# Performance work log

Hardware: AMD Instinct MI355X
Metric: run time of the kernel (lower is better)

The kernel has to match this reference:

```python
import jax, jax.numpy as jnp
import numpy as np

N_NODES = 15000
N_EDGES = 40000
N_GRAPHS = 750
D = 64
NODE_DIM = 32
EDGE_DIM = 16
NUM_CONV = 3
S2S_STEPS = 3


def setup_inputs() -> dict:
    key = jax.random.key(0)
    ks = jax.random.split(key, 24)
    s = 0.05
    inp = {
        'x': jax.random.normal(ks[0], (N_NODES, NODE_DIM), jnp.float32),
        'edge_attr': jax.random.uniform(ks[1], (N_EDGES, EDGE_DIM), jnp.float32),
        'edge_index': jax.random.randint(ks[2], (2, N_EDGES), 0, N_NODES),
        'batch': jnp.sort(jax.random.randint(ks[3], (N_NODES,), 0, N_GRAPHS)),
        # input projection
        'in_W': jax.random.normal(ks[4], (NODE_DIM, D)) * s,
        'in_b': jnp.zeros((D,)),
        # edge MLP -> per-edge DxD weights
        'e1_W': jax.random.normal(ks[5], (EDGE_DIM, D)) * s,
        'e1_b': jnp.zeros((D,)),
        'e2_W': jax.random.normal(ks[6], (D, D * D)) * s,
        'e2_b': jnp.zeros((D * D,)),
        'conv_b': jnp.zeros((D,)),
        # GRU (gate order r,z,n like torch)
        'gru_Wih': jax.random.normal(ks[7], (3 * D, D)) * s,
        'gru_Whh': jax.random.normal(ks[8], (3 * D, D)) * s,
        'gru_bih': jnp.zeros((3 * D,)),
        'gru_bhh': jnp.zeros((3 * D,)),
        # Set2Set LSTM (gate order i,f,g,o like torch), input 2D -> hidden D
        'lstm_Wih': jax.random.normal(ks[9], (4 * D, 2 * D)) * s,
        'lstm_Whh': jax.random.normal(ks[10], (4 * D, D)) * s,
        'lstm_bih': jnp.zeros((4 * D,)),
        'lstm_bhh': jnp.zeros((4 * D,)),
        # output MLP
        'out1_W': jax.random.normal(ks[11], (2 * D, 2 * D)) * s,
        'out1_b': jnp.zeros((2 * D,)),
        'out2_W': jax.random.normal(ks[12], (2 * D, 1)) * s,
        'out2_b': jnp.zeros((1,)),
    }
    return inp


def _gru_cell(m, h, Wih, Whh, bih, bhh):
    gi = m @ Wih.T + bih
    gh = h @ Whh.T + bhh
    ir, iz, inn = jnp.split(gi, 3, axis=-1)
    hr, hz, hn = jnp.split(gh, 3, axis=-1)
    r = jax.nn.sigmoid(ir + hr)
    z = jax.nn.sigmoid(iz + hz)
    n = jnp.tanh(inn + r * hn)
    return (1.0 - z) * n + z * h


def _lstm_cell(q, h, c, Wih, Whh, bih, bhh):
    g = q @ Wih.T + bih + h @ Whh.T + bhh
    i, f, gg, o = jnp.split(g, 4, axis=-1)
    c = jax.nn.sigmoid(f) * c + jax.nn.sigmoid(i) * jnp.tanh(gg)
    h = jax.nn.sigmoid(o) * jnp.tanh(c)
    return h, c


def reference(x, edge_attr, edge_index, batch,
              in_W, in_b, e1_W, e1_b, e2_W, e2_b, conv_b,
              gru_Wih, gru_Whh, gru_bih, gru_bhh,
              lstm_Wih, lstm_Whh, lstm_bih, lstm_bhh,
              out1_W, out1_b, out2_W, out2_b):
    src, dst = edge_index[0], edge_index[1]
    out = jax.nn.relu(x @ in_W + in_b)           # [N, D]
    h = out
    # edge-conditioned weights (edge_attr is constant across conv iters)
    W_e = (jax.nn.relu(edge_attr @ e1_W + e1_b) @ e2_W + e2_b).reshape(-1, D, D)  # [E, D, D]
    deg = jnp.maximum(jax.ops.segment_sum(jnp.ones((N_EDGES,), out.dtype), dst, N_NODES), 1.0)
    for _ in range(NUM_CONV):
        msg = jnp.einsum('ed,edf->ef', out[src], W_e)          # per-edge matmul
        agg = jax.ops.segment_sum(msg, dst, N_NODES) / deg[:, None]  # scatter-mean
        m = jax.nn.relu(agg + conv_b)
        h = _gru_cell(m, h, gru_Wih, gru_Whh, gru_bih, gru_bhh)
        out = h
    # Set2Set pooling
    q_star = jnp.zeros((N_GRAPHS, 2 * D), out.dtype)
    hl = jnp.zeros((N_GRAPHS, D), out.dtype)
    cl = jnp.zeros((N_GRAPHS, D), out.dtype)
    for _ in range(S2S_STEPS):
        hl, cl = _lstm_cell(q_star, hl, cl, lstm_Wih, lstm_Whh, lstm_bih, lstm_bhh)
        q = hl
        e = jnp.sum(out * q[batch], axis=-1)                    # [N]
        e = e - jax.ops.segment_max(e, batch, N_GRAPHS)[batch]
        ee = jnp.exp(e)
        a = ee / jax.ops.segment_sum(ee, batch, N_GRAPHS)[batch]
        r = jax.ops.segment_sum(a[:, None] * out, batch, N_GRAPHS)  # [G, D]
        q_star = jnp.concatenate([q, r], axis=-1)
    z = jax.nn.relu(q_star @ out1_W + out1_b) @ out2_W + out2_b
    return z
```

## Files before the change

### kernel.cpp

```cpp
#include <hip/hip_runtime.h>
#include <math.h>

#define N_NODES 15000
#define N_EDGES 40000
#define N_GRAPHS 750
#define N_TILES 938
#define N_TILES_PAD 944

typedef __attribute__((ext_vector_type(8))) short bf16x8;
typedef __attribute__((ext_vector_type(4))) float f32x4;

__device__ __forceinline__ float sigmoidf_(float x) { return 1.f / (1.f + expf(-x)); }

__device__ __forceinline__ unsigned short f2bf(float v) {
    unsigned u = __float_as_uint(v);
    unsigned r = (u + 0x7FFFu + ((u >> 16) & 1u)) >> 16;
    return (unsigned short)r;
}
__device__ __forceinline__ float bf2f(unsigned short b) {
    return __uint_as_float(((unsigned)b) << 16);
}


__global__ void tscan_kernel(const int* __restrict__ tcnt, int* __restrict__ tptr,
                             int* __restrict__ cursor) {
    __shared__ int buf[1024];
    int t = threadIdx.x;
    int v = (t < N_TILES) ? tcnt[t] : 0;
    buf[t] = v;
    __syncthreads();
    for (int ofs = 1; ofs < 1024; ofs <<= 1) {
        int a = (t >= ofs) ? buf[t - ofs] : 0;
        __syncthreads();
        buf[t] += a;
        __syncthreads();
    }
    int excl = buf[t] - v;
    if (t <= N_TILES_PAD) tptr[t] = excl;
    if (t < N_TILES) cursor[t] = excl;
}

__global__ void fillpack_kernel(const int* __restrict__ src, int* __restrict__ cursor,
                                int* __restrict__ edge_list,
                                const float* __restrict__ node_h,
                                unsigned short* __restrict__ Apack) {
    int b = blockIdx.x;
    int tid = threadIdx.x;
    if (b < 157) {
        int e = b * 256 + tid;
        if (e < N_EDGES) {
            int slot = atomicAdd(&cursor[src[e] >> 4], 1);
            edge_list[slot] = e;
        }
    } else {
        int nt = b - 157;
        for (int idx = tid; idx < 1024; idx += 256) {
            int kt = idx >> 9, lane = (idx >> 3) & 63, j = idx & 7;
            int quad = lane >> 4, m = lane & 15;
            int n = nt * 16 + m;
            float v = (n < N_NODES) ? node_h[(size_t)n * 64 + kt * 32 + quad * 8 + j] : 0.f;
            unsigned short hi = f2bf(v);
            Apack[nt * 2048 + kt * 1024 + lane * 8 + j] = hi;
            Apack[nt * 2048 + kt * 1024 + 512 + lane * 8 + j] = f2bf(v - bf2f(hi));
        }
    }
}

__global__ __launch_bounds__(256)
void prep_kernel(const float* __restrict__ x, const float* __restrict__ in_W,
                 const float* __restrict__ in_b, float* __restrict__ node_h,
                 const float* __restrict__ e2b,
                 const float* __restrict__ ea, const float* __restrict__ e1_W,
                 const float* __restrict__ e1_b, float* __restrict__ h1,
                 const float* __restrict__ e2W,
                 unsigned short* __restrict__ Bhi, unsigned short* __restrict__ Blo,
                 const float* __restrict__ lWih, const float* __restrict__ lWhh,
                 const float* __restrict__ gWih, const float* __restrict__ gWhh,
                 float* __restrict__ lWihT, float* __restrict__ lWhhT,
                 unsigned short* __restrict__ gWihP, unsigned short* __restrict__ gWhhP,
                 const int* __restrict__ batch, int* __restrict__ gptr,
                 const int* __restrict__ src, const int* __restrict__ dst,
                 int* __restrict__ tcnt, float* __restrict__ deg) {
    int b = blockIdx.x;
    int tid = threadIdx.x;
    if (b < 3750) {
        __shared__ float xs[4][32];
        int n0 = b * 4;
        if (tid < 128) xs[tid >> 5][tid & 31] = x[n0 * 32 + tid];
        __syncthreads();
        int nn = tid >> 6, f = tid & 63;
        float s = in_b[f];
        #pragma unroll
        for (int i = 0; i < 32; ++i) s += xs[nn][i] * in_W[i * 64 + f];
        node_h[(size_t)(n0 + nn) * 64 + f] = fmaxf(s, 0.f);
    } else if (b < 13750) {
        __shared__ float eas[4][16];
        int e0 = (b - 3750) * 4;
        if (tid < 64) eas[tid >> 4][tid & 15] = ea[e0 * 16 + tid];
        __syncthreads();
        int nn = tid >> 6, f = tid & 63;
        float s = e1_b[f];
        #pragma unroll
        for (int i = 0; i < 16; ++i) s += eas[nn][i] * e1_W[i * 64 + f];
        h1[(size_t)(e0 + nn) * 64 + f] = fmaxf(s, 0.f);
    } else if (b < 14806) {
        int idx = (b - 13750) * 256 + tid;
        int j = idx & 7, lane = (idx >> 3) & 63, kt = (idx >> 9) & 1;
        int rem = idx >> 10;
        int ct = rem % 33, ft = rem / 33;
        int d = kt * 32 + ((lane >> 4) << 3) + j;
        int m = lane & 15;
        float v;
        if (ct < 32) {
            int c = ct * 16 + m;
            int kk = c >> 3, fi = c & 7;
            v = e2W[(size_t)kk * 4096 + d * 64 + ft * 8 + fi];
        } else {
            v = (m < 8) ? e2b[d * 64 + ft * 8 + m] : 0.f;
        }
        unsigned short hi = f2bf(v);
        Bhi[idx] = hi;
        Blo[idx] = f2bf(v - bf2f(hi));
    } else if (b < 14998) {
        int idx = (b - 14806) * 256 + tid;
        if (idx < 32768) {
            int i = idx >> 8, r = idx & 255;
            lWihT[i * 256 + r] = lWih[r * 128 + i];
        } else if (idx < 49152) {
            int x2 = idx - 32768; int i = x2 >> 8, r = x2 & 255;
            lWhhT[i * 256 + r] = lWhh[r * 64 + i];
        }
    } else if (b < 15094) {
        int idx = (b - 14998) * 256 + tid;
        if (idx < 12288) {
            int j = idx & 7, lane = (idx >> 3) & 63, kt = (idx >> 9) & 1, ct = idx >> 10;
            int k = kt * 32 + ((lane >> 4) << 3) + j;
            int n = ct * 16 + (lane & 15);
            float v = gWih[n * 64 + k];
            unsigned short hi = f2bf(v);
            gWihP[idx] = hi;
            gWihP[12288 + idx] = f2bf(v - bf2f(hi));
        } else {
            int i2 = idx - 12288;
            int j = i2 & 7, lane = (i2 >> 3) & 63, kt = (i2 >> 9) & 1, ct = i2 >> 10;
            int k = kt * 32 + ((lane >> 4) << 3) + j;
            int n = ct * 16 + (lane & 15);
            float v = gWhh[n * 64 + k];
            unsigned short hi = f2bf(v);
            gWhhP[i2] = hi;
            gWhhP[12288 + i2] = f2bf(v - bf2f(hi));
        }
    } else if (b < 15153) {
        int n = (b - 15094) * 256 + tid;
        if (n < N_NODES) {
            int bb = batch[n];
            int pb = (n == 0) ? -1 : batch[n - 1];
            for (int g = pb + 1; g <= bb; ++g) gptr[g] = n;
            if (n == N_NODES - 1)
                for (int g = bb + 1; g <= N_GRAPHS; ++g) gptr[g] = N_NODES;
        }
    } else {
        int e = (b - 15153) * 256 + tid;
        if (e < N_EDGES) {
            atomicAdd(&tcnt[src[e] >> 4], 1);
            atomicAdd(&deg[dst[e]], 1.f);
        }
    }
}

__global__ __launch_bounds__(256, 4)
void conv_kernel(const unsigned short* __restrict__ Apack, const float* __restrict__ h1,
                 const unsigned short* __restrict__ Bhi, const unsigned short* __restrict__ Blo,
                 const int* __restrict__ tptr, const int* __restrict__ edge_list,
                 const int* __restrict__ src, const int* __restrict__ dst,
                 float* __restrict__ agg) {
    __shared__ float T_lds[16 * 548];
    int bid = blockIdx.x;
    int nt = bid % N_TILES_PAD, ft = bid / N_TILES_PAD;
    int n0 = nt * 16;
    int tid = threadIdx.x;
    int lane = tid & 63, wave = tid >> 6;
    int quad = lane >> 4, m = lane & 15;

    const unsigned short* ap = Apack + nt * 2048 + lane * 8;
    bf16x8 ahi[2], alo[2];
    ahi[0] = *(const bf16x8*)(ap);
    alo[0] = *(const bf16x8*)(ap + 512);
    ahi[1] = *(const bf16x8*)(ap + 1024);
    alo[1] = *(const bf16x8*)(ap + 1536);

    size_t base0 = (size_t)(ft * 33 + wave) * 1024 + lane * 8;
    const unsigned short* ph = Bhi + base0;
    const unsigned short* pl = Blo + base0;
    bf16x8 bh0 = *(const bf16x8*)(ph);
    bf16x8 bh1 = *(const bf16x8*)(ph + 512);
    bf16x8 bl0 = *(const bf16x8*)(pl);
    bf16x8 bl1 = *(const bf16x8*)(pl + 512);

    int nct = (wave == 0) ? 9 : 8;
    #pragma unroll 1
    for (int ci = 0; ci < nct; ++ci) {
        bf16x8 ch0 = bh0, ch1 = bh1, cl0 = bl0, cl1 = bl1;
        if (ci + 1 < nct) {
            const unsigned short* nh = ph + (size_t)(ci + 1) * 4096;
            const unsigned short* nl = pl + (size_t)(ci + 1) * 4096;
            bh0 = *(const bf16x8*)(nh);
            bh1 = *(const bf16x8*)(nh + 512);
            bl0 = *(const bf16x8*)(nl);
            bl1 = *(const bf16x8*)(nl + 512);
        }
        f32x4 accA = {0.f, 0.f, 0.f, 0.f};
        f32x4 accB = {0.f, 0.f, 0.f, 0.f};
        accA = __builtin_amdgcn_mfma_f32_16x16x32_bf16(ahi[0], ch0, accA, 0, 0, 0);
        accB = __builtin_amdgcn_mfma_f32_16x16x32_bf16(ahi[1], ch1, accB, 0, 0, 0);
        accA = __builtin_amdgcn_mfma_f32_16x16x32_bf16(alo[0], ch0, accA, 0, 0, 0);
        accB = __builtin_amdgcn_mfma_f32_16x16x32_bf16(alo[1], ch1, accB, 0, 0, 0);
        accA = __builtin_amdgcn_mfma_f32_16x16x32_bf16(ahi[0], cl0, accA, 0, 0, 0);
        accB = __builtin_amdgcn_mfma_f32_16x16x32_bf16(ahi[1], cl1, accB, 0, 0, 0);
        int ct = wave + ci * 4;
        int c = ct * 16 + m;
        int kk = c >> 3, fi = c & 7;
        #pragma unroll
        for (int r = 0; r < 4; ++r)
            T_lds[(quad * 4 + r) * 548 + fi * 68 + kk] = accA[r] + accB[r];
    }
    __syncthreads();

    int fi = tid & 7, slot = tid >> 3;
    int te0 = tptr[nt], te1 = tptr[nt + 1];
    for (int c = te0 + slot; c < te1; c += 64) {
        int c1 = c + 32;
        bool h2 = (c1 < te1);
        int e0 = edge_list[c];
        int e1 = h2 ? edge_list[c1] : e0;
        int nn0 = src[e0] - n0, nn1 = src[e1] - n0;
        const float* h0p = h1 + (size_t)e0 * 64;
        const float* h1p = h1 + (size_t)e1 * 64;
        const float* T0 = &T_lds[nn0 * 548 + fi * 68];
        const float* T1 = &T_lds[nn1 * 548 + fi * 68];
        float p00 = T0[64], p01 = 0.f;
        float p10 = T1[64], p11 = 0.f;
        #pragma unroll
        for (int k4 = 0; k4 < 64; k4 += 8) {
            float4 ha = *(const float4*)(h0p + k4);
            float4 ta = *(const float4*)(T0 + k4);
            float4 hb = *(const float4*)(h0p + k4 + 4);
            float4 tb = *(const float4*)(T0 + k4 + 4);
            float4 hc = *(const float4*)(h1p + k4);
            float4 tc = *(const float4*)(T1 + k4);
            float4 hd = *(const float4*)(h1p + k4 + 4);
            float4 td = *(const float4*)(T1 + k4 + 4);
            p00 += ha.x * ta.x + ha.y * ta.y + ha.z * ta.z + ha.w * ta.w;
            p01 += hb.x * tb.x + hb.y * tb.y + hb.z * tb.z + hb.w * tb.w;
            p10 += hc.x * tc.x + hc.y * tc.y + hc.z * tc.z + hc.w * tc.w;
            p11 += hd.x * td.x + hd.y * td.y + hd.z * td.z + hd.w * td.w;
        }
        atomicAdd(&agg[(size_t)dst[e0] * 64 + ft * 8 + fi], p00 + p01);
        if (h2) atomicAdd(&agg[(size_t)dst[e1] * 64 + ft * 8 + fi], p10 + p11);
    }
}

__global__ __launch_bounds__(256, 4)
void gru_kernel(float* __restrict__ node_h, float* __restrict__ agg,
                const float* __restrict__ deg, const float* __restrict__ conv_b,
                const unsigned short* __restrict__ WihP, const unsigned short* __restrict__ WhhP,
                const float* __restrict__ bih, const float* __restrict__ bhh,
                unsigned short* __restrict__ Apack, int want_pack) {
    __shared__ unsigned short m_bf[2][32][72];
    __shared__ unsigned short h_bf[2][32][72];
    __shared__ float h_s[32][68];
    __shared__ float hn_s[32][68];
    int n0 = blockIdx.x * 32;
    int tid = threadIdx.x;
    int lane = tid & 63, w = tid >> 6;
    int quad = lane >> 4, m16 = lane & 15;

    for (int i = tid; i < 2048; i += 256) {
        int c = i >> 6, f = i & 63;
        int n = n0 + c;
        float mv = 0.f, hv = 0.f;
        if (n < N_NODES) {
            float dg = fmaxf(deg[n], 1.f);
            mv = fmaxf(agg[(size_t)n * 64 + f] / dg + conv_b[f], 0.f);
            agg[(size_t)n * 64 + f] = 0.f;
            hv = node_h[(size_t)n * 64 + f];
        }
        unsigned short mh = f2bf(mv);
        m_bf[0][c][f] = mh; m_bf[1][c][f] = f2bf(mv - bf2f(mh));
        unsigned short hh = f2bf(hv);
        h_bf[0][c][f] = hh; h_bf[1][c][f] = f2bf(hv - bf2f(hh));
        h_s[c][f] = hv;
    }

    bf16x8 Bi[3][2][2], Bh[3][2][2];
    #pragma unroll
    for (int g = 0; g < 3; ++g)
        #pragma unroll
        for (int kt = 0; kt < 2; ++kt) {
            size_t base = ((size_t)((g * 4 + w) * 2 + kt) * 64 + lane) * 8;
            Bi[g][kt][0] = *(const bf16x8*)(WihP + base);
            Bi[g][kt][1] = *(const bf16x8*)(WihP + 12288 + base);
            Bh[g][kt][0] = *(const bf16x8*)(WhhP + base);
            Bh[g][kt][1] = *(const bf16x8*)(WhhP + 12288 + base);
        }
    int f = w * 16 + m16;
    float br_i = bih[f],       br_h = bhh[f];
    float bz_i = bih[64 + f],  bz_h = bhh[64 + f];
    float bn_i = bih[128 + f], bn_h = bhh[128 + f];
    __syncthreads();

    #pragma unroll 1
    for (int mt = 0; mt < 2; ++mt) {
        bf16x8 Am[2][2], Ah[2][2];
        #pragma unroll
        for (int kt = 0; kt < 2; ++kt) {
            Am[kt][0] = *(const bf16x8*)(&m_bf[0][mt * 16 + m16][kt * 32 + quad * 8]);
            Am[kt][1] = *(const bf16x8*)(&m_bf[1][mt * 16 + m16][kt * 32 + quad * 8]);
            Ah[kt][0] = *(const bf16x8*)(&h_bf[0][mt * 16 + m16][kt * 32 + quad * 8]);
            Ah[kt][1] = *(const bf16x8*)(&h_bf[1][mt * 16 + m16][kt * 32 + quad * 8]);
        }
        f32x4 ai[3], ah[3];
        #pragma unroll
        for (int g = 0; g < 3; ++g) { ai[g] = (f32x4){0.f,0.f,0.f,0.f}; ah[g] = (f32x4){0.f,0.f,0.f,0.f}; }
        #pragma unroll
        for (int g = 0; g < 3; ++g)
            #pragma unroll
            for (int kt = 0; kt < 2; ++kt) {
                ai[g] = __builtin_amdgcn_mfma_f32_16x16x32_bf16(Am[kt][0], Bi[g][kt][0], ai[g], 0, 0, 0);
                ai[g] = __builtin_amdgcn_mfma_f32_16x16x32_bf16(Am[kt][0], Bi[g][kt][1], ai[g], 0, 0, 0);
                ai[g] = __builtin_amdgcn_mfma_f32_16x16x32_bf16(Am[kt][1], Bi[g][kt][0], ai[g], 0, 0, 0);
                ah[g] = __builtin_amdgcn_mfma_f32_16x16x32_bf16(Ah[kt][0], Bh[g][kt][0], ah[g], 0, 0, 0);
                ah[g] = __builtin_amdgcn_mfma_f32_16x16x32_bf16(Ah[kt][0], Bh[g][kt][1], ah[g], 0, 0, 0);
                ah[g] = __builtin_amdgcn_mfma_f32_16x16x32_bf16(Ah[kt][1], Bh[g][kt][0], ah[g], 0, 0, 0);
            }
        #pragma unroll
        for (int r = 0; r < 4; ++r) {
            int node = mt * 16 + quad * 4 + r;
            float rr = sigmoidf_(ai[0][r] + br_i + ah[0][r] + br_h);
            float zz = sigmoidf_(ai[1][r] + bz_i + ah[1][r] + bz_h);
            float n2 = tanhf(ai[2][r] + bn_i + rr * (ah[2][r] + bn_h));
            float hnew = (1.f - zz) * n2 + zz * h_s[node][f];
            int n = n0 + node;
            if (n < N_NODES) node_h[(size_t)n * 64 + f] = hnew;
            hn_s[node][f] = hnew;
        }
    }
    if (want_pack) {
        __syncthreads();
        for (int idx = tid; idx < 2048; idx += 256) {
            int tt = idx >> 10, r2 = idx & 1023;
            int kt = r2 >> 9, ln = (r2 >> 3) & 63, j = r2 & 7;
            int q2 = ln >> 4, mm = ln & 15;
            float v = hn_s[tt * 16 + mm][kt * 32 + q2 * 8 + j];
            unsigned short hi = f2bf(v);
            size_t base = (size_t)(blockIdx.x * 2 + tt) * 2048 + kt * 1024 + ln * 8 + j;
            Apack[base] = hi;
            Apack[base + 512] = f2bf(v - bf2f(hi));
        }
    }
}

__global__ __launch_bounds__(128)
void s2s_kernel(const float* __restrict__ node_h, const int* __restrict__ gptr,
                const float* __restrict__ WihT, const float* __restrict__ WhhT,
                const float* __restrict__ bih, const float* __restrict__ bhh,
                const float* __restrict__ o1W, const float* __restrict__ o1b,
                const float* __restrict__ o2W, const float* __restrict__ o2b,
                float* __restrict__ z) {
    int g = blockIdx.x, tid = threadIdx.x;
    int f = tid & 63, half = tid >> 6;
    __shared__ float qs[128], hs[64], q[64], wts[128], gvs[4][64], racc_s[2][64];
    __shared__ float mred[2], sred[2], ored[2];
    if (half == 0) { qs[f] = 0.f; qs[64 + f] = 0.f; hs[f] = 0.f; }
    float c_t = 0.f;
    int nbeg = gptr[g], nend = gptr[g + 1];
    __syncthreads();
    for (int st = 0; st < 3; ++st) {
        #pragma unroll
        for (int gg = 0; gg < 2; ++gg) {
            int gate = half * 2 + gg;
            int row = gate * 64 + f;
            float s = bih[row] + bhh[row];
            #pragma unroll 8
            for (int i = 0; i < 128; ++i) s += qs[i] * WihT[i * 256 + row];
            #pragma unroll 8
            for (int i = 0; i < 64; ++i) s += hs[i] * WhhT[i * 256 + row];
            gvs[gate][f] = s;
        }
        __syncthreads();
        if (half == 0) {
            float c = sigmoidf_(gvs[1][f]) * c_t + sigmoidf_(gvs[0][f]) * tanhf(gvs[2][f]);
            float hn = sigmoidf_(gvs[3][f]) * tanhf(c);
            c_t = c;
            hs[f] = hn; q[f] = hn;
        }
        __syncthreads();
        float rm = -INFINITY, rs = 0.f, raccl = 0.f;
        for (int base = nbeg; base < nend; base += 128) {
            int n = base + tid;
            float e = -INFINITY;
            if (n < nend) {
                float s = 0.f;
                #pragma unroll 8
                for (int ff = 0; ff < 64; ++ff) s += node_h[(size_t)n * 64 + ff] * q[ff];
                e = s;
            }
            float cm = e;
            #pragma unroll
            for (int o = 32; o > 0; o >>= 1) cm = fmaxf(cm, __shfl_down(cm, o));
            if ((tid & 63) == 0) mred[half] = cm;
            __syncthreads();
            float bm = fmaxf(mred[0], mred[1]);
            float nm = fmaxf(rm, bm);
            float scale = (rm == -INFINITY) ? 0.f : expf(rm - nm);
            float wv = (n < nend) ? expf(e - nm) : 0.f;
            wts[tid] = wv;
            float cs = wv;
            #pragma unroll
            for (int o = 32; o > 0; o >>= 1) cs += __shfl_down(cs, o);
            if ((tid & 63) == 0) sred[half] = cs;
            __syncthreads();
            float bs = sred[0] + sred[1];
            float na = raccl * scale;
            int cnt2 = min(128, nend - base);
            int l0 = half * 64, l1 = min(l0 + 64, cnt2);
            for (int l = l0; l < l1; ++l) na += wts[l] * node_h[(size_t)(base + l) * 64 + f];
            raccl = na;
            rs = rs * scale + bs;
            rm = nm;
            __syncthreads();
        }
        racc_s[half][f] = raccl;
        __syncthreads();
        if (half == 0) {
            float r = (nend > nbeg) ? (racc_s[0][f] + racc_s[1][f]) / rs : 0.f;
            qs[f] = q[f];
            qs[64 + f] = r;
        }
        __syncthreads();
    }
    float sA = o1b[tid];
    #pragma unroll 8
    for (int i = 0; i < 128; ++i) sA += qs[i] * o1W[i * 128 + tid];
    float red = fmaxf(sA, 0.f) * o2W[tid];
    #pragma unroll
    for (int o = 32; o > 0; o >>= 1) red += __shfl_down(red, o);
    if ((tid & 63) == 0) ored[half] = red;
    __syncthreads();
    if (tid == 0) z[g] = ored[0] + ored[1] + o2b[0];
}

extern "C" void kernel_launch(void* const* d_in, const int* in_sizes, int n_in,
                              void* d_out, int out_size, void* d_ws, size_t ws_size,
                              hipStream_t stream) {
    const float* x         = (const float*)d_in[0];
    const float* edge_attr = (const float*)d_in[1];
    const int*   ei        = (const int*)d_in[2];
    const int*   batch     = (const int*)d_in[3];
    const float* in_W      = (const float*)d_in[4];
    const float* in_b      = (const float*)d_in[5];
    const float* e1_W      = (const float*)d_in[6];
    const float* e1_b      = (const float*)d_in[7];
    const float* e2_W      = (const float*)d_in[8];
    const float* e2_b      = (const float*)d_in[9];
    const float* conv_b    = (const float*)d_in[10];
    const float* gWih      = (const float*)d_in[11];
    const float* gWhh      = (const float*)d_in[12];
    const float* gbih      = (const float*)d_in[13];
    const float* gbhh      = (const float*)d_in[14];
    const float* lWih      = (const float*)d_in[15];
    const float* lWhh      = (const float*)d_in[16];
    const float* lbih      = (const float*)d_in[17];
    const float* lbhh      = (const float*)d_in[18];
    const float* o1W       = (const float*)d_in[19];
    const float* o1b       = (const float*)d_in[20];
    const float* o2W       = (const float*)d_in[21];
    const float* o2b       = (const float*)d_in[22];
    const int* src = ei;
    const int* dst = ei + N_EDGES;
    float* z = (float*)d_out;

    char* ws = (char*)d_ws;
    size_t off = 0;
    auto alloc = [&](size_t bytes) {
        void* p = ws + off;
        off = (off + bytes + 255) & ~(size_t)255;
        return p;
    };
    float* node_h   = (float*)alloc((size_t)N_NODES * 64 * 4);
    float* agg      = (float*)alloc((size_t)N_NODES * 64 * 4);
    float* h1       = (float*)alloc((size_t)N_EDGES * 64 * 4);
    unsigned short* Bhi = (unsigned short*)alloc((size_t)270336 * 2);
    unsigned short* Blo = (unsigned short*)alloc((size_t)270336 * 2);
    unsigned short* Apack = (unsigned short*)alloc((size_t)N_TILES_PAD * 2048 * 2);
    float* lWihT    = (float*)alloc(128 * 256 * 4);
    float* lWhhT    = (float*)alloc(64 * 256 * 4);
    unsigned short* gWihP = (unsigned short*)alloc(24576 * 2);
    unsigned short* gWhhP = (unsigned short*)alloc(24576 * 2);
    float* deg      = (float*)alloc(N_NODES * 4);
    int*   tcnt     = (int*)alloc((N_TILES + 2) * 4);
    int*   tcursor  = (int*)alloc((N_TILES + 2) * 4);
    int*   tptr     = (int*)alloc((N_TILES_PAD + 2) * 4);
    int*   edge_list= (int*)alloc(N_EDGES * 4);
    int*   gptr     = (int*)alloc((N_GRAPHS + 1) * 4);

    size_t degpad = ((size_t)N_NODES * 4 + 255) & ~(size_t)255;
    hipMemsetAsync(deg, 0, degpad + (N_TILES + 2) * 4, stream);
    hipMemsetAsync(agg, 0, (size_t)N_NODES * 64 * 4, stream);

    prep_kernel<<<15310, 256, 0, stream>>>(x, in_W, in_b, node_h, e2_b,
                                           edge_attr, e1_W, e1_b, h1,
                                           e2_W, Bhi, Blo,
                                           lWih, lWhh, gWih, gWhh,
                                           lWihT, lWhhT, gWihP, gWhhP,
                                           batch, gptr, src, dst, tcnt, deg);
    tscan_kernel<<<1, 1024, 0, stream>>>(tcnt, tptr, tcursor);
    fillpack_kernel<<<157 + N_TILES_PAD, 256, 0, stream>>>(src, tcursor, edge_list,
                                                           node_h, Apack);

    for (int it = 0; it < 3; ++it) {
        conv_kernel<<<N_TILES_PAD * 8, 256, 0, stream>>>(Apack, h1, Bhi, Blo,
                                                         tptr, edge_list, src, dst, agg);
        gru_kernel<<<469, 256, 0, stream>>>(node_h, agg, deg, conv_b,
                                            gWihP, gWhhP, gbih, gbhh,
                                            Apack, (it < 2) ? 1 : 0);
    }
    s2s_kernel<<<N_GRAPHS, 128, 0, stream>>>(node_h, gptr, lWihT, lWhhT, lbih, lbhh,
                                             o1W, o1b, o2W, o2b, z);
}
```

Before: 437.0 us.

## Prefetch first edge batch in conv, batch prep blocks, widen Set2Set block

Three separate changes. The conv kernel loads the first edge chunk (edge ids, src/dst and the first h1 slice) before the MFMA loop, so those global loads overlap with the matrix compute instead of following the barrier. The prep kernel makes each block handle 16 nodes or 32 edges, cutting the block count roughly fourfold at the cost of extra in-block barriers. The s2s kernel moves to 256 threads, one wave per LSTM gate, and processes 256 nodes per softmax chunk, which adds reduction slots and leaves half the threads idle in the output MLP.

```diff
diff --git a/kernel.cpp b/kernel.cpp
--- a/kernel.cpp
+++ b/kernel.cpp
@@ -83,28 +83,39 @@
                  int* __restrict__ tcnt, float* __restrict__ deg) {
     int b = blockIdx.x;
     int tid = threadIdx.x;
-    if (b < 3750) {
+    if (b < 938) {
         __shared__ float xs[4][32];
-        int n0 = b * 4;
-        if (tid < 128) xs[tid >> 5][tid & 31] = x[n0 * 32 + tid];
-        __syncthreads();
-        int nn = tid >> 6, f = tid & 63;
-        float s = in_b[f];
-        #pragma unroll
-        for (int i = 0; i < 32; ++i) s += xs[nn][i] * in_W[i * 64 + f];
-        node_h[(size_t)(n0 + nn) * 64 + f] = fmaxf(s, 0.f);
-    } else if (b < 13750) {
+        int n0 = b * 16;
+        for (int g2 = 0; g2 < 4; ++g2) {
+            int nb = n0 + g2 * 4;
+            __syncthreads();
+            if (tid < 128) {
+                int xi = nb * 32 + tid;
+                xs[tid >> 5][tid & 31] = (xi < N_NODES * 32) ? x[xi] : 0.f;
+            }
+            __syncthreads();
+            int nn = tid >> 6, f = tid & 63;
+            float s = in_b[f];
+            #pragma unroll
+            for (int i = 0; i < 32; ++i) s += xs[nn][i] * in_W[i * 64 + f];
+            if (nb + nn < N_NODES) node_h[(size_t)(nb + nn) * 64 + f] = fmaxf(s, 0.f);
+        }
+    } else if (b < 2188) {
         __shared__ float eas[4][16];
-        int e0 = (b - 3750) * 4;
-        if (tid < 64) eas[tid >> 4][tid & 15] = ea[e0 * 16 + tid];
-        __syncthreads();
-        int nn = tid >> 6, f = tid & 63;
-        float s = e1_b[f];
-        #pragma unroll
-        for (int i = 0; i < 16; ++i) s += eas[nn][i] * e1_W[i * 64 + f];
-        h1[(size_t)(e0 + nn) * 64 + f] = fmaxf(s, 0.f);
-    } else if (b < 14806) {
-        int idx = (b - 13750) * 256 + tid;
+        int e0 = (b - 938) * 32;
+        for (int g2 = 0; g2 < 8; ++g2) {
+            int eb = e0 + g2 * 4;
+            __syncthreads();
+            if (tid < 64) eas[tid >> 4][tid & 15] = ea[eb * 16 + tid];
+            __syncthreads();
+            int nn = tid >> 6, f = tid & 63;
+            float s = e1_b[f];
+            #pragma unroll
+            for (int i = 0; i < 16; ++i) s += eas[nn][i] * e1_W[i * 64 + f];
+            h1[(size_t)(eb + nn) * 64 + f] = fmaxf(s, 0.f);
+        }
+    } else if (b < 3244) {
+        int idx = (b - 2188) * 256 + tid;
         int j = idx & 7, lane = (idx >> 3) & 63, kt = (idx >> 9) & 1;
         int rem = idx >> 10;
         int ct = rem % 33, ft = rem / 33;
@@ -121,8 +132,8 @@
         unsigned short hi = f2bf(v);
         Bhi[idx] = hi;
         Blo[idx] = f2bf(v - bf2f(hi));
-    } else if (b < 14998) {
-        int idx = (b - 14806) * 256 + tid;
+    } else if (b < 3436) {
+        int idx = (b - 3244) * 256 + tid;
         if (idx < 32768) {
             int i = idx >> 8, r = idx & 255;
             lWihT[i * 256 + r] = lWih[r * 128 + i];
@@ -130,8 +141,8 @@
             int x2 = idx - 32768; int i = x2 >> 8, r = x2 & 255;
             lWhhT[i * 256 + r] = lWhh[r * 64 + i];
         }
-    } else if (b < 15094) {
-        int idx = (b - 14998) * 256 + tid;
+    } else if (b < 3532) {
+        int idx = (b - 3436) * 256 + tid;
         if (idx < 12288) {
             int j = idx & 7, lane = (idx >> 3) & 63, kt = (idx >> 9) & 1, ct = idx >> 10;
             int k = kt * 32 + ((lane >> 4) << 3) + j;
@@ -150,8 +161,8 @@
             gWhhP[i2] = hi;
             gWhhP[12288 + i2] = f2bf(v - bf2f(hi));
         }
-    } else if (b < 15153) {
-        int n = (b - 15094) * 256 + tid;
+    } else if (b < 3591) {
+        int n = (b - 3532) * 256 + tid;
         if (n < N_NODES) {
             int bb = batch[n];
             int pb = (n == 0) ? -1 : batch[n - 1];
@@ -160,7 +171,7 @@
                 for (int g = bb + 1; g <= N_GRAPHS; ++g) gptr[g] = N_NODES;
         }
     } else {
-        int e = (b - 15153) * 256 + tid;
+        int e = (b - 3591) * 256 + tid;
         if (e < N_EDGES) {
             atomicAdd(&tcnt[src[e] >> 4], 1);
             atomicAdd(&deg[dst[e]], 1.f);
@@ -182,6 +193,24 @@
     int lane = tid & 63, wave = tid >> 6;
     int quad = lane >> 4, m = lane & 15;
 
+    int te0 = tptr[nt], te1 = tptr[nt + 1];
+    int fi = tid & 7, slot = tid >> 3;
+    int cA = te0 + slot, cB = cA + 32;
+    int eA = (cA < te1) ? edge_list[cA] : -1;
+    int eB = (cB < te1) ? edge_list[cB] : -1;
+    int sA_ = 0, dA_ = 0, sB_ = 0, dB_ = 0;
+    float4 pa0 = make_float4(0.f, 0.f, 0.f, 0.f), pa1 = pa0, pb0 = pa0, pb1 = pa0;
+    if (eA >= 0) {
+        sA_ = src[eA]; dA_ = dst[eA];
+        pa0 = *(const float4*)(h1 + (size_t)eA * 64);
+        pa1 = *(const float4*)(h1 + (size_t)eA * 64 + 4);
+    }
+    if (eB >= 0) {
+        sB_ = src[eB]; dB_ = dst[eB];
+        pb0 = *(const float4*)(h1 + (size_t)eB * 64);
+        pb1 = *(const float4*)(h1 + (size_t)eB * 64 + 4);
+    }
+
     const unsigned short* ap = Apack + nt * 2048 + lane * 8;
     bf16x8 ahi[2], alo[2];
     ahi[0] = *(const bf16x8*)(ap);
@@ -219,16 +248,50 @@
         accB = __builtin_amdgcn_mfma_f32_16x16x32_bf16(ahi[1], cl1, accB, 0, 0, 0);
         int ct = wave + ci * 4;
         int c = ct * 16 + m;
-        int kk = c >> 3, fi = c & 7;
+        int kk = c >> 3, fo = c & 7;
         #pragma unroll
         for (int r = 0; r < 4; ++r)
-            T_lds[(quad * 4 + r) * 548 + fi * 68 + kk] = accA[r] + accB[r];
+            T_lds[(quad * 4 + r) * 548 + fo * 68 + kk] = accA[r] + accB[r];
     }
     __syncthreads();
 
-    int fi = tid & 7, slot = tid >> 3;
-    int te0 = tptr[nt], te1 = tptr[nt + 1];
-    for (int c = te0 + slot; c < te1; c += 64) {
+    if (eA >= 0) {
+        int nn0 = sA_ - n0;
+        int nn1 = (eB >= 0 ? sB_ : sA_) - n0;
+        const float* h0p = h1 + (size_t)eA * 64;
+        const float* h1p = h1 + (size_t)(eB >= 0 ? eB : eA) * 64;
+        const float* T0 = &T_lds[nn0 * 548 + fi * 68];
+        const float* T1 = &T_lds[nn1 * 548 + fi * 68];
+        float p00 = T0[64], p01 = 0.f, p10 = T1[64], p11 = 0.f;
+        {
+            float4 ta = *(const float4*)(T0);
+            float4 tb = *(const float4*)(T0 + 4);
+            float4 tc = *(const float4*)(T1);
+            float4 td = *(const float4*)(T1 + 4);
+            p00 += pa0.x * ta.x + pa0.y * ta.y + pa0.z * ta.z + pa0.w * ta.w;
+            p01 += pa1.x * tb.x + pa1.y * tb.y + pa1.z * tb.z + pa1.w * tb.w;
+            p10 += pb0.x * tc.x + pb0.y * tc.y + pb0.z * tc.z + pb0.w * tc.w;
+            p11 += pb1.x * td.x + pb1.y * td.y + pb1.z * td.z + pb1.w * td.w;
+        }
+        #pragma unroll
+        for (int k4 = 8; k4 < 64; k4 += 8) {
+            float4 ha = *(const float4*)(h0p + k4);
+            float4 ta = *(const float4*)(T0 + k4);
+            float4 hb = *(const float4*)(h0p + k4 + 4);
+            float4 tb = *(const float4*)(T0 + k4 + 4);
+            float4 hc = *(const float4*)(h1p + k4);
+            float4 tc = *(const float4*)(T1 + k4);
+            float4 hd = *(const float4*)(h1p + k4 + 4);
+            float4 td = *(const float4*)(T1 + k4 + 4);
+            p00 += ha.x * ta.x + ha.y * ta.y + ha.z * ta.z + ha.w * ta.w;
+            p01 += hb.x * tb.x + hb.y * tb.y + hb.z * tb.z + hb.w * tb.w;
+            p10 += hc.x * tc.x + hc.y * tc.y + hc.z * tc.z + hc.w * tc.w;
+            p11 += hd.x * td.x + hd.y * td.y + hd.z * td.z + hd.w * td.w;
+        }
+        atomicAdd(&agg[(size_t)dA_ * 64 + ft * 8 + fi], p00 + p01);
+        if (eB >= 0) atomicAdd(&agg[(size_t)dB_ * 64 + ft * 8 + fi], p10 + p11);
+    }
+    for (int c = cA + 64; c < te1; c += 64) {
         int c1 = c + 32;
         bool h2 = (c1 < te1);
         int e0 = edge_list[c];
@@ -238,8 +301,7 @@
         const float* h1p = h1 + (size_t)e1 * 64;
         const float* T0 = &T_lds[nn0 * 548 + fi * 68];
         const float* T1 = &T_lds[nn1 * 548 + fi * 68];
-        float p00 = T0[64], p01 = 0.f;
-        float p10 = T1[64], p11 = 0.f;
+        float p00 = T0[64], p01 = 0.f, p10 = T1[64], p11 = 0.f;
         #pragma unroll
         for (int k4 = 0; k4 < 64; k4 += 8) {
             float4 ha = *(const float4*)(h0p + k4);
@@ -360,7 +422,7 @@
     }
 }
 
-__global__ __launch_bounds__(128)
+__global__ __launch_bounds__(256)
 void s2s_kernel(const float* __restrict__ node_h, const int* __restrict__ gptr,
                 const float* __restrict__ WihT, const float* __restrict__ WhhT,
                 const float* __restrict__ bih, const float* __restrict__ bhh,
@@ -368,49 +430,47 @@
                 const float* __restrict__ o2W, const float* __restrict__ o2b,
                 float* __restrict__ z) {
     int g = blockIdx.x, tid = threadIdx.x;
-    int f = tid & 63, half = tid >> 6;
-    __shared__ float qs[128], hs[64], q[64], wts[128], gvs[4][64], racc_s[2][64];
-    __shared__ float mred[2], sred[2], ored[2];
-    if (half == 0) { qs[f] = 0.f; qs[64 + f] = 0.f; hs[f] = 0.f; }
+    int f = tid & 63, q = tid >> 6;
+    __shared__ float qs[128], hs[64], qv[64], wts[256], gvs[4][64], racc_s[4][64];
+    __shared__ float mred[4], sred[4], ored[2];
+    if (q == 0) { qs[f] = 0.f; qs[64 + f] = 0.f; hs[f] = 0.f; }
     float c_t = 0.f;
     int nbeg = gptr[g], nend = gptr[g + 1];
     __syncthreads();
     for (int st = 0; st < 3; ++st) {
-        #pragma unroll
-        for (int gg = 0; gg < 2; ++gg) {
-            int gate = half * 2 + gg;
-            int row = gate * 64 + f;
+        {
+            int row = q * 64 + f;
             float s = bih[row] + bhh[row];
             #pragma unroll 8
             for (int i = 0; i < 128; ++i) s += qs[i] * WihT[i * 256 + row];
             #pragma unroll 8
             for (int i = 0; i < 64; ++i) s += hs[i] * WhhT[i * 256 + row];
-            gvs[gate][f] = s;
-        }
-        __syncthreads();
-        if (half == 0) {
+            gvs[q][f] = s;
+        }
+        __syncthreads();
+        if (q == 0) {
             float c = sigmoidf_(gvs[1][f]) * c_t + sigmoidf_(gvs[0][f]) * tanhf(gvs[2][f]);
             float hn = sigmoidf_(gvs[3][f]) * tanhf(c);
             c_t = c;
-            hs[f] = hn; q[f] = hn;
+            hs[f] = hn; qv[f] = hn;
         }
         __syncthreads();
         float rm = -INFINITY, rs = 0.f, raccl = 0.f;
-        for (int base = nbeg; base < nend; base += 128) {
+        for (int base = nbeg; base < nend; base += 256) {
             int n = base + tid;
             float e = -INFINITY;
             if (n < nend) {
                 float s = 0.f;
                 #pragma unroll 8
-                for (int ff = 0; ff < 64; ++ff) s += node_h[(size_t)n * 64 + ff] * q[ff];
+                for (int ff = 0; ff < 64; ++ff) s += node_h[(size_t)n * 64 + ff] * qv[ff];
                 e = s;
             }
             float cm = e;
             #pragma unroll
             for (int o = 32; o > 0; o >>= 1) cm = fmaxf(cm, __shfl_down(cm, o));
-            if ((tid & 63) == 0) mred[half] = cm;
-            __syncthreads();
-            float bm = fmaxf(mred[0], mred[1]);
+            if ((tid & 63) == 0) mred[q] = cm;
+            __syncthreads();
+            float bm = fmaxf(fmaxf(mred[0], mred[1]), fmaxf(mred[2], mred[3]));
             float nm = fmaxf(rm, bm);
             float scale = (rm == -INFINITY) ? 0.f : expf(rm - nm);
             float wv = (n < nend) ? expf(e - nm) : 0.f;
@@ -418,34 +478,38 @@
             float cs = wv;
             #pragma unroll
             for (int o = 32; o > 0; o >>= 1) cs += __shfl_down(cs, o);
-            if ((tid & 63) == 0) sred[half] = cs;
-            __syncthreads();
-            float bs = sred[0] + sred[1];
+            if ((tid & 63) == 0) sred[q] = cs;
+            __syncthreads();
+            float bs = (sred[0] + sred[1]) + (sred[2] + sred[3]);
             float na = raccl * scale;
-            int cnt2 = min(128, nend - base);
-            int l0 = half * 64, l1 = min(l0 + 64, cnt2);
+            int cnt2 = min(256, nend - base);
+            int l0 = q * 64, l1 = min(l0 + 64, cnt2);
             for (int l = l0; l < l1; ++l) na += wts[l] * node_h[(size_t)(base + l) * 64 + f];
             raccl = na;
             rs = rs * scale + bs;
             rm = nm;
             __syncthreads();
         }
-        racc_s[half][f] = raccl;
-        __syncthreads();
-        if (half == 0) {
-            float r = (nend > nbeg) ? (racc_s[0][f] + racc_s[1][f]) / rs : 0.f;
-            qs[f] = q[f];
+        racc_s[q][f] = raccl;
+        __syncthreads();
+        if (q == 0) {
+            float r = (nend > nbeg)
+                    ? ((racc_s[0][f] + racc_s[1][f]) + (racc_s[2][f] + racc_s[3][f])) / rs
+                    : 0.f;
+            qs[f] = qv[f];
             qs[64 + f] = r;
         }
         __syncthreads();
     }
-    float sA = o1b[tid];
-    #pragma unroll 8
-    for (int i = 0; i < 128; ++i) sA += qs[i] * o1W[i * 128 + tid];
-    float red = fmaxf(sA, 0.f) * o2W[tid];
-    #pragma unroll
-    for (int o = 32; o > 0; o >>= 1) red += __shfl_down(red, o);
-    if ((tid & 63) == 0) ored[half] = red;
+    if (tid < 128) {
+        float sA = o1b[tid];
+        #pragma unroll 8
+        for (int i = 0; i < 128; ++i) sA += qs[i] * o1W[i * 128 + tid];
+        float red = fmaxf(sA, 0.f) * o2W[tid];
+        #pragma unroll
+        for (int o = 32; o > 0; o >>= 1) red += __shfl_down(red, o);
+        if ((tid & 63) == 0) ored[tid >> 6] = red;
+    }
     __syncthreads();
     if (tid == 0) z[g] = ored[0] + ored[1] + o2b[0];
 }
@@ -508,12 +572,12 @@
     hipMemsetAsync(deg, 0, degpad + (N_TILES + 2) * 4, stream);
     hipMemsetAsync(agg, 0, (size_t)N_NODES * 64 * 4, stream);
 
-    prep_kernel<<<15310, 256, 0, stream>>>(x, in_W, in_b, node_h, e2_b,
-                                           edge_attr, e1_W, e1_b, h1,
-                                           e2_W, Bhi, Blo,
-                                           lWih, lWhh, gWih, gWhh,
-                                           lWihT, lWhhT, gWihP, gWhhP,
-                                           batch, gptr, src, dst, tcnt, deg);
+    prep_kernel<<<3748, 256, 0, stream>>>(x, in_W, in_b, node_h, e2_b,
+                                          edge_attr, e1_W, e1_b, h1,
+                                          e2_W, Bhi, Blo,
+                                          lWih, lWhh, gWih, gWhh,
+                                          lWihT, lWhhT, gWihP, gWhhP,
+                                          batch, gptr, src, dst, tcnt, deg);
     tscan_kernel<<<1, 1024, 0, stream>>>(tcnt, tptr, tcursor);
     fillpack_kernel<<<157 + N_TILES_PAD, 256, 0, stream>>>(src, tcursor, edge_list,
                                                            node_h, Apack);
@@ -525,6 +589,6 @@
                                             gWihP, gWhhP, gbih, gbhh,
                                             Apack, (it < 2) ? 1 : 0);
     }
-    s2s_kernel<<<N_GRAPHS, 128, 0, stream>>>(node_h, gptr, lWihT, lWhhT, lbih, lbhh,
+    s2s_kernel<<<N_GRAPHS, 256, 0, stream>>>(node_h, gptr, lWihT, lWhhT, lbih, lbhh,
                                              o1W, o1b, o2W, o2b, z);
 }
```

Measured after the change: 430.3 us. Within noise of the previous version (-1.5%).
